# Optimization experiments

Measured on AMD Instinct MI355X. Metric: run time of the kernel, lower is better.

Reference implementation:

```python
import jax, jax.numpy as jnp
import numpy as np

# --- SLAYER hyperparameters (from netParams) ---
THETA = 10.0        # spike threshold
TAU_SR = 10.0       # SRM alpha-kernel time constant (ms)
TAU_RHO = 1.0       # surrogate-gradient width
SCALE_RHO = 1.0     # surrogate-gradient scale
TS = 1.0            # simulation step (ms)
T_SAMPLE = 300      # number of time steps
K_LEN = 64          # truncated SRM kernel length

N_BATCH, N_IN, N_HID, N_OUT = 128, 784, 410, 10


def srm_kernel():
    # SRM-alpha kernel eps(t) = (t/tau) * exp(1 - t/tau), sampled at Ts, eps(0)=0
    t = jnp.arange(K_LEN, dtype=jnp.float32) * TS
    return (t / TAU_SR) * jnp.exp(1.0 - t / TAU_SR)


def psp(x):
    # Causal FIR filtering along time: out[t] = sum_k eps[k] * x[t-k]
    # x: [N, C, T]
    n, c, t = x.shape
    kern = srm_kernel()
    lhs = x.reshape(n * c, 1, t)
    rhs = kern[::-1].reshape(1, 1, K_LEN)  # flip: conv_general_dilated is cross-correlation
    out = jax.lax.conv_general_dilated(
        lhs, rhs, window_strides=(1,), padding=[(K_LEN - 1, 0)],
        dimension_numbers=("NCH", "OIH", "NCH"))
    return out.reshape(n, c, t)


@jax.custom_vjp
def spike_fn(u):
    # Heaviside threshold with surrogate gradient rho(u) = (scale/tau) * exp(-|u-theta|/tau)
    return (u >= THETA).astype(u.dtype)

def _spike_fwd(u):
    return spike_fn(u), u

def _spike_bwd(u, g):
    return (g * (SCALE_RHO / TAU_RHO) * jnp.exp(-jnp.abs(u - THETA) / TAU_RHO),)

spike_fn.defvjp(_spike_fwd, _spike_bwd)


def setup_inputs() -> dict:
    key = jax.random.key(0)
    k1, k2, k3, k4 = jax.random.split(key, 4)
    img = jax.random.uniform(k1, (N_BATCH, N_IN), dtype=jnp.float32)
    rand_u = jax.random.uniform(k2, (N_BATCH, N_IN, T_SAMPLE), dtype=jnp.float32)
    W1 = jax.random.normal(k3, (N_HID, N_IN), dtype=jnp.float32)
    W2 = jax.random.normal(k4, (N_OUT, N_HID), dtype=jnp.float32)
    return {"img": img, "rand_u": rand_u, "W1": W1, "W2": W2}


def reference(img, rand_u, W1, W2):
    # Poisson spike encoding: spike whenever uniform noise < pixel intensity
    s0 = (rand_u < img[:, :, None]).astype(jnp.float32)        # [N, 784, T]
    # fc1 (dense over spatial features, shared over time) -> psp -> spike
    a1 = jnp.einsum("nit,oi->not", s0, W1)                     # [N, 410, T]
    s1 = spike_fn(psp(a1))
    # fc2 -> psp -> spike
    a2 = jnp.einsum("nht,oh->not", s1, W2)                     # [N, 10, T]
    s2 = spike_fn(psp(a2))
    return s2
```

## Files before the change

### kernel.cpp

```cpp
#include <hip/hip_runtime.h>
#include <cstdint>
#include <cstddef>

#define N_B 128
#define N_I 784
#define N_H 410
#define N_O 10
#define TT  300
#define KL  64
#define NK  832
#define NKS 13
#define NTILES 26
#define NDIG 4
#define NKS2 7
#define S1_TILE 4800
#define S1_NSTRIDE 134400
#define SEGL 19
#define SEGL2 10
#define NWG1 (NTILES * N_B)
#define WPX  (NWG1 / 8)
#define PACKBLK (5 * NKS * N_B)
#define PREPBLK (NDIG * NTILES * NKS + NDIG * NKS2)

typedef int v4i __attribute__((ext_vector_type(4)));

__global__ void k_prep(const float* __restrict__ rand_u, const float* __restrict__ img,
                       const float* __restrict__ W1, const float* __restrict__ W2,
                       uint8_t* __restrict__ s0b, v4i* __restrict__ Bf,
                       v4i* __restrict__ Bf2) {
  int bid0 = blockIdx.x;
  int lane = threadIdx.x;
  if (bid0 < PACKBLK) {
    int t  = (bid0 % 5) * 64 + lane;
    int w2 = (bid0 / 5) % NKS;
    int n  = bid0 / (5 * NKS);
    if (t >= TT) return;
    const float* rb = rand_u + (size_t)n * N_I * TT + t;
    const float* ib = img + (size_t)n * N_I;
    uint8_t* dst = s0b + ((size_t)n * TT + t) * NK + w2 * 64;
    int kb = w2 * 64;
    #pragma unroll
    for (int g = 0; g < 4; ++g) {
      uint32_t wd[4];
      #pragma unroll
      for (int q = 0; q < 4; ++q) {
        uint32_t v = 0;
        #pragma unroll
        for (int b = 0; b < 4; ++b) {
          int i = kb + g * 16 + q * 4 + b;
          float r = (i < N_I) ? rb[(size_t)i * TT] : 2.0f;
          float p = (i < N_I) ? ib[i] : 0.0f;
          v |= (r < p ? 1u : 0u) << (8 * b);
        }
        wd[q] = v;
      }
      v4i o; o[0] = (int)wd[0]; o[1] = (int)wd[1]; o[2] = (int)wd[2]; o[3] = (int)wd[3];
      *(v4i*)(dst + g * 16) = o;
    }
    return;
  }
  int bid = bid0 - PACKBLK;
  if (bid < NDIG * NTILES * NKS) {
    int ks   = bid % NKS;
    int rest = bid / NKS;
    int nt   = rest % NTILES;
    int d    = rest / NTILES;
    int o     = nt * 16 + (lane & 15);
    int kbase = ks * 64 + (lane >> 4) * 16;
    uint32_t wds[4] = {0, 0, 0, 0};
    for (int j = 0; j < 16; ++j) {
      int k = kbase + j;
      int dig = 0;
      if (o < N_H && k < N_I) {
        double w = (double)W1[(size_t)o * N_I + k];
        int r = (int)llround(w * 268435456.0);
        for (int dd = 0; dd <= d; ++dd) {
          dig = (int)(int8_t)(uint8_t)(r & 255);
          r = (r - dig) >> 8;
        }
      }
      wds[j >> 2] |= ((uint32_t)(uint8_t)(int8_t)dig) << (8 * (j & 3));
    }
    v4i v; v[0] = (int)wds[0]; v[1] = (int)wds[1]; v[2] = (int)wds[2]; v[3] = (int)wds[3];
    Bf[(size_t)bid * 64 + lane] = v;
  } else {
    int b2 = bid - NDIG * NTILES * NKS;
    int ks = b2 % NKS2, d = b2 / NKS2;
    int o     = lane & 15;
    int kbase = ks * 64 + (lane >> 4) * 16;
    uint32_t wds[4] = {0, 0, 0, 0};
    for (int j = 0; j < 16; ++j) {
      int k = kbase + j;
      int dig = 0;
      if (o < N_O && k < N_H) {
        double w = (double)W2[(size_t)o * N_H + k];
        int r = (int)llround(w * 268435456.0);
        for (int dd = 0; dd <= d; ++dd) {
          dig = (int)(int8_t)(uint8_t)(r & 255);
          r = (r - dig) >> 8;
        }
      }
      wds[j >> 2] |= ((uint32_t)(uint8_t)(int8_t)dig) << (8 * (j & 3));
    }
    v4i v; v[0] = (int)wds[0]; v[1] = (int)wds[1]; v[2] = (int)wds[2]; v[3] = (int)wds[3];
    Bf2[(size_t)b2 * 64 + lane] = v;
  }
}

__global__ __launch_bounds__(256) void k_fused2(const uint8_t* __restrict__ s0b,
                                                const v4i* __restrict__ Bf,
                                                uint8_t* __restrict__ s1) {
  __shared__ double tile[TT][17];
  int tid = threadIdx.x;
  int wave = tid >> 6, lane = tid & 63;
  int bid = blockIdx.x;
  int sw = (bid & 7) * WPX + (bid >> 3);
  int n = sw / NTILES, nt = sw % NTILES;
  int lrow = lane & 15, quad = lane >> 4;

  const v4i* bb = Bf + (size_t)nt * NKS * 64 + lane;
  const size_t dstr = (size_t)NTILES * NKS * 64;
  const uint8_t* an = s0b + (size_t)n * TT * NK + quad * 16;
  const uint8_t* ap[5];
  #pragma unroll
  for (int m = 0; m < 5; ++m) {
    int rr = wave * 80 + m * 16 + lrow;
    if (rr > TT - 1) rr = TT - 1;
    ap[m] = an + (size_t)rr * NK;
  }

  v4i acc[5][NDIG];
  #pragma unroll
  for (int m = 0; m < 5; ++m)
    #pragma unroll
    for (int d = 0; d < NDIG; ++d) { acc[m][d][0]=0; acc[m][d][1]=0; acc[m][d][2]=0; acc[m][d][3]=0; }

  v4i a[3][5], b[2][4];
  #pragma unroll
  for (int m = 0; m < 5; ++m) a[0][m] = *(const v4i*)(ap[m]);
  #pragma unroll
  for (int d = 0; d < NDIG; ++d) b[0][d] = bb[(size_t)d * dstr];
  #pragma unroll
  for (int m = 0; m < 5; ++m) a[1][m] = *(const v4i*)(ap[m] + 64);
  #pragma unroll
  for (int d = 0; d < NDIG; ++d) b[1][d] = bb[(size_t)d * dstr + 64];

  #pragma unroll
  for (int ks = 0; ks < NKS; ++ks) {
    if (ks + 2 < NKS) {
      #pragma unroll
      for (int m = 0; m < 5; ++m)
        a[(ks + 2) % 3][m] = *(const v4i*)(ap[m] + (ks + 2) * 64);
    }
    #pragma unroll
    for (int m = 0; m < 5; ++m)
      #pragma unroll
      for (int d = 0; d < NDIG; ++d)
        acc[m][d] = __builtin_amdgcn_mfma_i32_16x16x64_i8(a[ks % 3][m], b[ks & 1][d], acc[m][d], 0, 0, 0);
    if (ks + 2 < NKS) {
      #pragma unroll
      for (int d = 0; d < NDIG; ++d)
        b[(ks + 2) & 1][d] = bb[(size_t)d * dstr + (ks + 2) * 64];
    }
  }

  #pragma unroll
  for (int m5 = 0; m5 < 5; ++m5)
    #pragma unroll
    for (int r = 0; r < 4; ++r) {
      int m = wave * 80 + m5 * 16 + quad * 4 + r;
      if (m < TT) {
        double v = (double)acc[m5][0][r]
                 + 256.0      * (double)acc[m5][1][r]
                 + 65536.0    * (double)acc[m5][2][r]
                 + 16777216.0 * (double)acc[m5][3][r];
        tile[m][lrow] = v;
      }
    }
  __syncthreads();

  {
    int col = tid & 15;
    int seg = tid >> 4;
    int T0 = seg * SEGL;
    const double q   = exp(-0.1);
    const double q64 = exp(-6.4);
    const double cS  = (exp(1.0) / 10.0) * (1.0 / 268435456.0);
    const double thr = 10.0 / cS;
    double s1a = 0.0, s2a = 0.0, s1b = 0.0, s2b = 0.0;
    uint8_t* sb = s1 + (size_t)n * S1_NSTRIDE + (size_t)nt * S1_TILE + col;
    if (wave == 0) {
      int Wc = T0 - 63; if (Wc < 0) Wc = 0;
      for (int j = 0; j < 63; ++j) {
        int t = T0 - 63 + j;
        int tc = (t < 0) ? 0 : t;
        double xa = (t >= 0) ? tile[tc][col] : 0.0;
        s2a = q * (s2a + s1a);
        s1a = q * s1a + xa;
      }
      for (int j = 0; j < SEGL; ++j) {
        int t = T0 + j;
        int tc = (t > TT - 1) ? TT - 1 : t;
        int tb = t - 64;
        int tbc = (tb < 0) ? 0 : tb;
        double xa = tile[tc][col];
        double xb = (tb >= Wc) ? tile[tbc][col] : 0.0;
        s2b = q * (s2b + s1b);
        s1b = q * s1b + xb;
        s2a = q * (s2a + s1a);
        s1a = q * s1a + xa;
        double z = s2a - q64 * (s2b + 64.0 * s1b);
        if (t < TT) sb[(size_t)t * 16] = (z >= thr) ? 1 : 0;
      }
    } else {
      int W0 = T0 - 63;
      #pragma unroll 7
      for (int j = 0; j < 63; ++j) {
        double xa = tile[W0 + j][col];
        s2a = q * (s2a + s1a);
        s1a = q * s1a + xa;
      }
      {
        double xa = tile[T0][col];
        s2a = q * (s2a + s1a);
        s1a = q * s1a + xa;
        sb[(size_t)T0 * 16] = (s2a >= thr) ? 1 : 0;
      }
      #pragma unroll 6
      for (int j = 1; j < SEGL; ++j) {
        int t = T0 + j;
        int tc = (t > TT - 1) ? TT - 1 : t;
        double xa = tile[tc][col];
        double xb = tile[t - 64][col];
        s2b = q * (s2b + s1b);
        s1b = q * s1b + xb;
        s2a = q * (s2a + s1a);
        s1a = q * s1a + xa;
        double z = s2a - q64 * (s2b + 64.0 * s1b);
        if (t < TT) sb[(size_t)t * 16] = (z >= thr) ? 1 : 0;
      }
    }
  }
}

__global__ __launch_bounds__(256) void k_l2f(const uint8_t* __restrict__ s1,
                                             const v4i* __restrict__ Bf2,
                                             float* __restrict__ out) {
  __shared__ double tile2[TT][17];
  int tid = threadIdx.x;
  int wave = tid >> 6, lane = tid & 63;
  int half = blockIdx.x, n = blockIdx.y;
  int lrow = lane & 15, quad = lane >> 4;
  const uint8_t* s1n = s1 + (size_t)n * S1_NSTRIDE;
  for (int mt = wave; mt < 19; mt += 4) {
    int m0 = mt * 16;
    int trow = m0 + lrow; if (trow > TT - 1) trow = TT - 1;
    v4i acc[NDIG];
    #pragma unroll
    for (int d = 0; d < NDIG; ++d) { acc[d][0]=0; acc[d][1]=0; acc[d][2]=0; acc[d][3]=0; }
    for (int ks = 0; ks < NKS2; ++ks) {
      v4i af = *(const v4i*)(s1n + (size_t)(ks * 4 + quad) * S1_TILE + (size_t)trow * 16);
      #pragma unroll
      for (int d = 0; d < NDIG; ++d) {
        v4i bf = Bf2[(size_t)(d * NKS2 + ks) * 64 + lane];
        acc[d] = __builtin_amdgcn_mfma_i32_16x16x64_i8(af, bf, acc[d], 0, 0, 0);
      }
    }
    #pragma unroll
    for (int r = 0; r < 4; ++r) {
      int m = m0 + quad * 4 + r;
      if (m < TT && lrow < N_O) {
        double v = (double)acc[0][r]
                 + 256.0      * (double)acc[1][r]
                 + 65536.0    * (double)acc[2][r]
                 + 16777216.0 * (double)acc[3][r];
        tile2[m][lrow] = v;
      }
    }
  }
  __syncthreads();

  {
    int col = tid & 15;
    int seg = half * 16 + (tid >> 4);
    int T0 = seg * SEGL2;
    int Wc = T0 - 63; if (Wc < 0) Wc = 0;
    const double q   = exp(-0.1);
    const double q64 = exp(-6.4);
    const double cS  = (exp(1.0) / 10.0) * (1.0 / 268435456.0);
    const double thr = 10.0 / cS;
    double s1a = 0.0, s2a = 0.0, s1b = 0.0, s2b = 0.0;
    float* ob = out + (size_t)n * N_O * TT + (size_t)col * TT;
    for (int j = 0; j < 63; ++j) {
      int t = T0 - 63 + j;
      int tc = (t < 0) ? 0 : t;
      tc = (tc > TT - 1) ? TT - 1 : tc;
      double xa = (t >= 0 && t < TT) ? tile2[tc][col] : 0.0;
      s2a = q * (s2a + s1a);
      s1a = q * s1a + xa;
    }
    for (int j = 0; j < SEGL2; ++j) {
      int t = T0 + j;
      int tc = (t > TT - 1) ? TT - 1 : t;
      int tb = t - 64;
      int tbc = (tb < 0) ? 0 : tb;
      tbc = (tbc > TT - 1) ? TT - 1 : tbc;
      double xa = tile2[tc][col];
      double xb = (tb >= Wc) ? tile2[tbc][col] : 0.0;
      s2b = q * (s2b + s1b);
      s1b = q * s1b + xb;
      s2a = q * (s2a + s1a);
      s1a = q * s1a + xa;
      double z = s2a - q64 * (s2b + 64.0 * s1b);
      if (t < TT && col < N_O) ob[t] = (z >= thr) ? 1.0f : 0.0f;
    }
  }
}

extern "C" void kernel_launch(void* const* d_in, const int* in_sizes, int n_in,
                              void* d_out, int out_size, void* d_ws, size_t ws_size,
                              hipStream_t stream) {
  const float* img   = (const float*)d_in[0];
  const float* randu = (const float*)d_in[1];
  const float* W1    = (const float*)d_in[2];
  const float* W2    = (const float*)d_in[3];
  float* out = (float*)d_out;

  char* ws = (char*)d_ws;
  size_t off = 0;
  auto alloc = [&](size_t bytes) -> void* {
    void* p = ws + off;
    off = (off + bytes + 511) & ~(size_t)511;
    return p;
  };
  uint8_t*  s0b = (uint8_t*) alloc((size_t)N_B * TT * NK);
  v4i*      Bf  = (v4i*)     alloc((size_t)NDIG * NTILES * NKS * 64 * 16);
  v4i*      Bf2 = (v4i*)     alloc((size_t)NDIG * NKS2 * 64 * 16);
  uint8_t*  s1  = (uint8_t*) alloc((size_t)N_B * S1_NSTRIDE);
  if (off > ws_size) return;

  k_prep  <<<dim3(PACKBLK + PREPBLK), 64, 0, stream>>>(randu, img, W1, W2, s0b, Bf, Bf2);
  k_fused2<<<dim3(NWG1), 256, 0, stream>>>(s0b, Bf, s1);
  k_l2f   <<<dim3(2, N_B), 256, 0, stream>>>(s1, Bf2, out);
}
```

Baseline: 339.9 us.

## Stage GEMM operands through LDS with async global_load_lds double buffering

Replaces direct global-to-register operand loads in the fused int8 MFMA GEMM with asynchronous global_load_lds copies into double-buffered LDS staging. Manual vmcnt/lgkmcnt waits and sched barriers pipeline the copies about two k-steps ahead while the MFMAs run. The epilogue tile now aliases the staging buffer, and a barrier is added before it is reused. The goal is to hide global latency and cut register pressure from the three-deep register prefetch. The cost is a 72 KB LDS footprint, which may lower occupancy, and fragile hand-counted wait values.

```diff
diff --git a/kernel.cpp b/kernel.cpp
--- a/kernel.cpp
+++ b/kernel.cpp
@@ -19,10 +19,17 @@
 #define SEGL2 10
 #define NWG1 (NTILES * N_B)
 #define WPX  (NWG1 / 8)
+#define DBYTES (NTILES * NKS * 1024)
 #define PACKBLK (5 * NKS * N_B)
 #define PREPBLK (NDIG * NTILES * NKS + NDIG * NKS2)
 
 typedef int v4i __attribute__((ext_vector_type(4)));
+
+__device__ __forceinline__ void glds16(const void* g, void* l) {
+  __builtin_amdgcn_global_load_lds(
+      (const __attribute__((address_space(1))) uint32_t*)g,
+      (__attribute__((address_space(3))) uint32_t*)l, 16, 0, 0);
+}
 
 __global__ void k_prep(const float* __restrict__ rand_u, const float* __restrict__ img,
                        const float* __restrict__ W1, const float* __restrict__ W2,
@@ -110,7 +117,11 @@
 __global__ __launch_bounds__(256) void k_fused2(const uint8_t* __restrict__ s0b,
                                                 const v4i* __restrict__ Bf,
                                                 uint8_t* __restrict__ s1) {
-  __shared__ double tile[TT][17];
+  __shared__ __align__(16) uint8_t smem[73728];
+  uint8_t* bufA = smem;
+  uint8_t* bufB = smem + 40960;
+  double (*tile)[17] = (double (*)[17])smem;
+
   int tid = threadIdx.x;
   int wave = tid >> 6, lane = tid & 63;
   int bid = blockIdx.x;
@@ -118,16 +129,35 @@
   int n = sw / NTILES, nt = sw % NTILES;
   int lrow = lane & 15, quad = lane >> 4;
 
-  const v4i* bb = Bf + (size_t)nt * NKS * 64 + lane;
-  const size_t dstr = (size_t)NTILES * NKS * 64;
-  const uint8_t* an = s0b + (size_t)n * TT * NK + quad * 16;
-  const uint8_t* ap[5];
-  #pragma unroll
-  for (int m = 0; m < 5; ++m) {
-    int rr = wave * 80 + m * 16 + lrow;
-    if (rr > TT - 1) rr = TT - 1;
-    ap[m] = an + (size_t)rr * NK;
-  }
+  const uint8_t* an0 = s0b + (size_t)n * TT * NK;
+  int arow = wave * 80 + (lane & 15);
+  int acolg = (lane >> 4) * 16;
+  const uint8_t* bfb = (const uint8_t*)Bf + (size_t)nt * NKS * 1024 + (size_t)lane * 16;
+
+  auto STAGE = [&](int k, int par) {
+    uint8_t* ad = bufA + par * 20480 + wave * 5120;
+    #pragma unroll
+    for (int c = 0; c < 5; ++c) {
+      int r = arow + c * 16; if (r > TT - 1) r = TT - 1;
+      glds16(an0 + (size_t)r * NK + (size_t)k * 64 + acolg, ad + c * 1024);
+    }
+    uint8_t* bd = bufB + par * 16384 + wave * 4096;
+    #pragma unroll
+    for (int d = 0; d < NDIG; ++d)
+      glds16(bfb + (size_t)d * DBYTES + (size_t)k * 1024, bd + d * 1024);
+  };
+  auto LDA = [&](int par, v4i* a) {
+    const uint8_t* base = bufA + par * 20480 + wave * 5120 + quad * 256 + lrow * 16;
+    #pragma unroll
+    for (int m = 0; m < 5; ++m)
+      a[m] = *(const v4i*)(base + m * 1024);
+  };
+  auto LDB = [&](int par, v4i* b) {
+    const uint8_t* base = bufB + par * 16384 + wave * 4096 + lane * 16;
+    #pragma unroll
+    for (int d = 0; d < NDIG; ++d)
+      b[d] = *(const v4i*)(base + d * 1024);
+  };
 
   v4i acc[5][NDIG];
   #pragma unroll
@@ -135,34 +165,38 @@
     #pragma unroll
     for (int d = 0; d < NDIG; ++d) { acc[m][d][0]=0; acc[m][d][1]=0; acc[m][d][2]=0; acc[m][d][3]=0; }
 
-  v4i a[3][5], b[2][4];
-  #pragma unroll
-  for (int m = 0; m < 5; ++m) a[0][m] = *(const v4i*)(ap[m]);
-  #pragma unroll
-  for (int d = 0; d < NDIG; ++d) b[0][d] = bb[(size_t)d * dstr];
-  #pragma unroll
-  for (int m = 0; m < 5; ++m) a[1][m] = *(const v4i*)(ap[m] + 64);
-  #pragma unroll
-  for (int d = 0; d < NDIG; ++d) b[1][d] = bb[(size_t)d * dstr + 64];
+  STAGE(0, 0);
+  STAGE(1, 1);
+  asm volatile("s_waitcnt vmcnt(9)" ::: "memory");
+  v4i acur[5], bcur[NDIG], anxt[5], bnxt[NDIG];
+  LDA(0, acur); LDB(0, bcur);
+  asm volatile("s_waitcnt lgkmcnt(0)" ::: "memory");
+  __builtin_amdgcn_sched_barrier(0);
+  STAGE(2, 0);
 
   #pragma unroll
   for (int ks = 0; ks < NKS; ++ks) {
-    if (ks + 2 < NKS) {
-      #pragma unroll
-      for (int m = 0; m < 5; ++m)
-        a[(ks + 2) % 3][m] = *(const v4i*)(ap[m] + (ks + 2) * 64);
-    }
+    if (ks < NKS - 2) { asm volatile("s_waitcnt vmcnt(9)" ::: "memory"); }
+    else              { asm volatile("s_waitcnt vmcnt(0)" ::: "memory"); }
+    int pn = (ks + 1) & 1;
+    if (ks < NKS - 1) { LDA(pn, anxt); LDB(pn, bnxt); }
     #pragma unroll
     for (int m = 0; m < 5; ++m)
       #pragma unroll
       for (int d = 0; d < NDIG; ++d)
-        acc[m][d] = __builtin_amdgcn_mfma_i32_16x16x64_i8(a[ks % 3][m], b[ks & 1][d], acc[m][d], 0, 0, 0);
-    if (ks + 2 < NKS) {
-      #pragma unroll
-      for (int d = 0; d < NDIG; ++d)
-        b[(ks + 2) & 1][d] = bb[(size_t)d * dstr + (ks + 2) * 64];
-    }
-  }
+        acc[m][d] = __builtin_amdgcn_mfma_i32_16x16x64_i8(acur[m], bcur[d], acc[m][d], 0, 0, 0);
+    asm volatile("s_waitcnt lgkmcnt(0)" ::: "memory");
+    __builtin_amdgcn_sched_barrier(0);
+    if (ks < NKS - 3) STAGE(ks + 3, (ks + 3) & 1);
+    if (ks < NKS - 1) {
+      #pragma unroll
+      for (int m = 0; m < 5; ++m) acur[m] = anxt[m];
+      #pragma unroll
+      for (int d = 0; d < NDIG; ++d) bcur[d] = bnxt[d];
+    }
+  }
+
+  __syncthreads();
 
   #pragma unroll
   for (int m5 = 0; m5 < 5; ++m5)
```

Result: faster. 313.6 us (-7.7%).

## Stage A operand through LDS with async global_load_lds triple buffering

Applied to the files above, without the earlier changes.

Replaces the per-thread global register loads of the spike-matrix A operand with direct global-to-LDS async loads into a 3-stage ring buffer. Explicit vmcnt waits and sched barriers order the loads against the MFMA loop, and the LDS region is reused for the epilogue tile. The intent is to cut VGPR pressure, allowing 2 blocks per CU, and to hide global latency. The cost is a larger shared-memory footprint, hand-counted waitcnts that are fragile if the load count changes, and an extra barrier.

```diff
diff --git a/kernel.cpp b/kernel.cpp
--- a/kernel.cpp
+++ b/kernel.cpp
@@ -24,6 +24,12 @@
 
 typedef int v4i __attribute__((ext_vector_type(4)));
 
+__device__ __forceinline__ void glds16(const void* g, void* l) {
+  __builtin_amdgcn_global_load_lds(
+      (const __attribute__((address_space(1))) uint32_t*)g,
+      (__attribute__((address_space(3))) uint32_t*)l, 16, 0, 0);
+}
+
 __global__ void k_prep(const float* __restrict__ rand_u, const float* __restrict__ img,
                        const float* __restrict__ W1, const float* __restrict__ W2,
                        uint8_t* __restrict__ s0b, v4i* __restrict__ Bf,
@@ -107,10 +113,13 @@
   }
 }
 
-__global__ __launch_bounds__(256) void k_fused2(const uint8_t* __restrict__ s0b,
-                                                const v4i* __restrict__ Bf,
-                                                uint8_t* __restrict__ s1) {
-  __shared__ double tile[TT][17];
+__global__ __launch_bounds__(256, 2) void k_fused2(const uint8_t* __restrict__ s0b,
+                                                   const v4i* __restrict__ Bf,
+                                                   uint8_t* __restrict__ s1) {
+  __shared__ __align__(16) uint8_t smem[61440];
+  uint8_t* bufA = smem;
+  double (*tile)[17] = (double (*)[17])smem;
+
   int tid = threadIdx.x;
   int wave = tid >> 6, lane = tid & 63;
   int bid = blockIdx.x;
@@ -118,16 +127,20 @@
   int n = sw / NTILES, nt = sw % NTILES;
   int lrow = lane & 15, quad = lane >> 4;
 
+  const uint8_t* an0 = s0b + (size_t)n * TT * NK;
+  int arow = wave * 80 + (lane & 15);
+  int acolg = (lane >> 4) * 16;
   const v4i* bb = Bf + (size_t)nt * NKS * 64 + lane;
   const size_t dstr = (size_t)NTILES * NKS * 64;
-  const uint8_t* an = s0b + (size_t)n * TT * NK + quad * 16;
-  const uint8_t* ap[5];
-  #pragma unroll
-  for (int m = 0; m < 5; ++m) {
-    int rr = wave * 80 + m * 16 + lrow;
-    if (rr > TT - 1) rr = TT - 1;
-    ap[m] = an + (size_t)rr * NK;
-  }
+
+  auto STAGE_A = [&](int k, int par) {
+    uint8_t* ad = bufA + par * 20480 + wave * 5120;
+    #pragma unroll
+    for (int c = 0; c < 5; ++c) {
+      int r = arow + c * 16; if (r > TT - 1) r = TT - 1;
+      glds16(an0 + (size_t)r * NK + (size_t)k * 64 + acolg, ad + c * 1024);
+    }
+  };
 
   v4i acc[5][NDIG];
   #pragma unroll
@@ -135,34 +148,43 @@
     #pragma unroll
     for (int d = 0; d < NDIG; ++d) { acc[m][d][0]=0; acc[m][d][1]=0; acc[m][d][2]=0; acc[m][d][3]=0; }
 
-  v4i a[3][5], b[2][4];
-  #pragma unroll
-  for (int m = 0; m < 5; ++m) a[0][m] = *(const v4i*)(ap[m]);
+  STAGE_A(0, 0);
+  STAGE_A(1, 1);
+  STAGE_A(2, 2);
+  v4i b[2][NDIG];
   #pragma unroll
   for (int d = 0; d < NDIG; ++d) b[0][d] = bb[(size_t)d * dstr];
   #pragma unroll
-  for (int m = 0; m < 5; ++m) a[1][m] = *(const v4i*)(ap[m] + 64);
-  #pragma unroll
   for (int d = 0; d < NDIG; ++d) b[1][d] = bb[(size_t)d * dstr + 64];
 
   #pragma unroll
   for (int ks = 0; ks < NKS; ++ks) {
+    if (ks <= NKS - 3)      { asm volatile("s_waitcnt vmcnt(18)" ::: "memory"); }
+    else if (ks == NKS - 2) { asm volatile("s_waitcnt vmcnt(13)" ::: "memory"); }
+    else                    { asm volatile("s_waitcnt vmcnt(4)"  ::: "memory"); }
+    v4i a[5];
+    {
+      const uint8_t* base = bufA + (ks % 3) * 20480 + wave * 5120 + quad * 256 + lrow * 16;
+      #pragma unroll
+      for (int m = 0; m < 5; ++m) a[m] = *(const v4i*)(base + m * 1024);
+    }
+    #pragma unroll
+    for (int m = 0; m < 5; ++m)
+      #pragma unroll
+      for (int d = 0; d < NDIG; ++d)
+        acc[m][d] = __builtin_amdgcn_mfma_i32_16x16x64_i8(a[m], b[ks & 1][d], acc[m][d], 0, 0, 0);
+    asm volatile("s_waitcnt lgkmcnt(0)" ::: "memory");
+    __builtin_amdgcn_sched_barrier(0);
     if (ks + 2 < NKS) {
       #pragma unroll
-      for (int m = 0; m < 5; ++m)
-        a[(ks + 2) % 3][m] = *(const v4i*)(ap[m] + (ks + 2) * 64);
-    }
-    #pragma unroll
-    for (int m = 0; m < 5; ++m)
-      #pragma unroll
       for (int d = 0; d < NDIG; ++d)
-        acc[m][d] = __builtin_amdgcn_mfma_i32_16x16x64_i8(a[ks % 3][m], b[ks & 1][d], acc[m][d], 0, 0, 0);
-    if (ks + 2 < NKS) {
-      #pragma unroll
-      for (int d = 0; d < NDIG; ++d)
-        b[(ks + 2) & 1][d] = bb[(size_t)d * dstr + (ks + 2) * 64];
-    }
-  }
+        b[ks & 1][d] = bb[(size_t)d * dstr + (size_t)(ks + 2) * 64];
+    }
+    __builtin_amdgcn_sched_barrier(0);
+    if (ks + 3 < NKS) STAGE_A(ks + 3, ks % 3);
+  }
+
+  __syncthreads();
 
   #pragma unroll
   for (int m5 = 0; m5 < 5; ++m5)
```

Result: faster. 320.5 us (-5.7%).
